# Kernel tuning notes

Hardware: AMD Instinct MI355X
Metric: run time of the kernel (lower is better)

Reference implementation:

```python
import jax, jax.numpy as jnp
import numpy as np

N_X = 50000      # real nodes
N_MOTIF = 10000  # motif nodes
N = N_X + N_MOTIF
E = 1_920_000    # edges (avg degree 32)
NFEAT = 512
NHID = 256
PAD_N = 65536


def setup_inputs() -> dict:
    key = jax.random.key(0)
    ks = jax.random.split(key, 12)
    x = jax.random.normal(ks[0], (N_X, NFEAT), dtype=jnp.float32)
    motif_emb = jax.random.normal(ks[1], (N_MOTIF, NFEAT), dtype=jnp.float32)
    adj_rows = jax.random.randint(ks[2], (E,), 0, N)
    adj_cols = jax.random.randint(ks[3], (E,), 0, N)
    adj_vals = jax.random.uniform(ks[4], (E,), dtype=jnp.float32)
    # unique scatter positions (torch output[pos_idx]=x with distinct indices)
    pos_idx = jax.random.permutation(ks[5], PAD_N)[:N_X]
    # GraphConvolution params (pygcn style: support = x@W; out = spmm(adj, support) + b)
    s1 = 1.0 / np.sqrt(NHID)
    w1 = jax.random.uniform(ks[6], (NFEAT, NHID), minval=-s1, maxval=s1, dtype=jnp.float32)
    b1 = jax.random.uniform(ks[7], (NHID,), minval=-s1, maxval=s1, dtype=jnp.float32)
    w2 = jax.random.uniform(ks[8], (NHID, NHID), minval=-s1, maxval=s1, dtype=jnp.float32)
    b2 = jax.random.uniform(ks[9], (NHID,), minval=-s1, maxval=s1, dtype=jnp.float32)
    w3 = jax.random.uniform(ks[10], (NHID, NHID), minval=-s1, maxval=s1, dtype=jnp.float32)
    b3 = jax.random.uniform(ks[11], (NHID,), minval=-s1, maxval=s1, dtype=jnp.float32)
    return {"x": x, "motif_emb": motif_emb, "adj_rows": adj_rows, "adj_cols": adj_cols,
            "adj_vals": adj_vals, "pos_idx": pos_idx, "pad_n": PAD_N,
            "w1": w1, "b1": b1, "w2": w2, "b2": b2, "w3": w3, "b3": b3}


def _gcn_layer(h, rows, cols, vals, w, b):
    support = h @ w                                   # [N, nhid]
    msgs = vals[:, None] * support[cols]              # [E, nhid]
    agg = jax.ops.segment_sum(msgs, rows, num_segments=N)  # spmm(adj, support)
    return jax.nn.relu(agg + b)


def reference(x, motif_emb, adj_rows, adj_cols, adj_vals, pos_idx, pad_n,
              w1, b1, w2, b2, w3, b3):
    h = jnp.concatenate((x, motif_emb), axis=0)       # [N, nfeat]
    h = _gcn_layer(h, adj_rows, adj_cols, adj_vals, w1, b1)
    # dropout is identity in eval mode
    h = _gcn_layer(h, adj_rows, adj_cols, adj_vals, w2, b2)
    h = _gcn_layer(h, adj_rows, adj_cols, adj_vals, w3, b3)
    h = h[:N_X]                                       # drop motif nodes
    output = jnp.zeros((pad_n, h.shape[1]), dtype=h.dtype)
    output = output.at[pos_idx].set(h)                # irregular scatter-assign
    return output
```

## Files before the change

kernel.cpp:

```cpp
#include <hip/hip_runtime.h>

#define N_TOTAL 60000
#define N_X     50000
#define N_EDGE  1920000
#define NFEAT   512
#define NHID    256
#define SLOTS   96

typedef __attribute__((ext_vector_type(8))) short bf16x8;
typedef __attribute__((ext_vector_type(4))) float f32x4;
typedef __attribute__((ext_vector_type(4))) unsigned u32x4;

__device__ __forceinline__ unsigned short f2bf(float f) {
    unsigned u = __float_as_uint(f);
    unsigned r = (u + 0x7FFFu + ((u >> 16) & 1u)) >> 16;
    return (unsigned short)r;
}
__device__ __forceinline__ float bf_lo(unsigned u) { return __uint_as_float(u << 16); }
__device__ __forceinline__ float bf_hi(unsigned u) { return __uint_as_float(u & 0xFFFF0000u); }

__global__ __launch_bounds__(256)
void cvt_w_all_kernel(const float* __restrict__ w1, const float* __restrict__ w2,
                      const float* __restrict__ w3, short* __restrict__ w1T,
                      short* __restrict__ w2T, short* __restrict__ w3T)
{
    int n = blockIdx.x;
    for (int k = threadIdx.x; k < NFEAT; k += 256)
        w1T[(size_t)n * NFEAT + k] = (short)f2bf(w1[(size_t)k * NHID + n]);
    for (int k = threadIdx.x; k < NHID; k += 256)
        w2T[(size_t)n * NHID + k] = (short)f2bf(w2[(size_t)k * NHID + n]);
    for (int k = threadIdx.x; k < NHID; k += 256)
        w3T[(size_t)n * NHID + k] = (short)f2bf(w3[(size_t)k * NHID + n]);
}

#define LDA 40

template<bool AF32>
__global__ __launch_bounds__(256)
void gemm_bt_kernel(const float* __restrict__ Af, const float* __restrict__ A2f, int split,
                    const short* __restrict__ Ab, const short* __restrict__ BT,
                    short* __restrict__ C, int M, int K)
{
    __shared__ short As[128 * LDA];
    __shared__ short Bs[128 * LDA];
    const int t    = threadIdx.x;
    const int lane = t & 63;
    const int wave = t >> 6;
    const int wm   = wave & 1;
    const int wn   = wave >> 1;
    const int l16  = lane & 15;
    const int quad = lane >> 4;
    const int bm   = blockIdx.x * 128;
    const int bn   = blockIdx.y * 128;

    f32x4 acc[4][4] = {};

    const int srow = t >> 2;
    const int sch  = t & 3;
    const int frow = t >> 1;
    const int fh   = t & 1;

    for (int kk = 0; kk < K; kk += 32) {
        if (AF32) {
            int row = bm + frow;
            float4 v0 = {}, v1 = {}, v2 = {}, v3 = {};
            if (row < M) {
                const float* src = (row < split) ? (Af + (size_t)row * K)
                                                 : (A2f + (size_t)(row - split) * K);
                const float4* p = (const float4*)(src + kk + fh * 16);
                v0 = p[0]; v1 = p[1]; v2 = p[2]; v3 = p[3];
            }
            short* dst = &As[frow * LDA + fh * 16];
            short tmp[16] = {
                (short)f2bf(v0.x), (short)f2bf(v0.y), (short)f2bf(v0.z), (short)f2bf(v0.w),
                (short)f2bf(v1.x), (short)f2bf(v1.y), (short)f2bf(v1.z), (short)f2bf(v1.w),
                (short)f2bf(v2.x), (short)f2bf(v2.y), (short)f2bf(v2.z), (short)f2bf(v2.w),
                (short)f2bf(v3.x), (short)f2bf(v3.y), (short)f2bf(v3.z), (short)f2bf(v3.w)};
            *(bf16x8*)(dst)     = *(const bf16x8*)&tmp[0];
            *(bf16x8*)(dst + 8) = *(const bf16x8*)&tmp[8];
        } else {
            bf16x8 va0 = {}, va1 = {};
            int r0 = bm + srow, r1 = bm + srow + 64;
            if (r0 < M) va0 = *(const bf16x8*)(Ab + (size_t)r0 * K + kk + sch * 8);
            if (r1 < M) va1 = *(const bf16x8*)(Ab + (size_t)r1 * K + kk + sch * 8);
            *(bf16x8*)&As[srow * LDA + sch * 8]        = va0;
            *(bf16x8*)&As[(srow + 64) * LDA + sch * 8] = va1;
        }
        {
            bf16x8 vb0 = *(const bf16x8*)(BT + (size_t)(bn + srow) * K + kk + sch * 8);
            bf16x8 vb1 = *(const bf16x8*)(BT + (size_t)(bn + srow + 64) * K + kk + sch * 8);
            *(bf16x8*)&Bs[srow * LDA + sch * 8]        = vb0;
            *(bf16x8*)&Bs[(srow + 64) * LDA + sch * 8] = vb1;
        }
        __syncthreads();

        bf16x8 af[4], bfr[4];
        #pragma unroll
        for (int i = 0; i < 4; i++) {
            af[i]  = *(const bf16x8*)&As[(wm * 64 + i * 16 + l16) * LDA + quad * 8];
            bfr[i] = *(const bf16x8*)&Bs[(wn * 64 + i * 16 + l16) * LDA + quad * 8];
        }
        #pragma unroll
        for (int i = 0; i < 4; i++)
            #pragma unroll
            for (int j = 0; j < 4; j++)
                acc[i][j] = __builtin_amdgcn_mfma_f32_16x16x32_bf16(af[i], bfr[j], acc[i][j], 0, 0, 0);
        __syncthreads();
    }

    #pragma unroll
    for (int i = 0; i < 4; i++) {
        #pragma unroll
        for (int r = 0; r < 4; r++) {
            int row = bm + wm * 64 + i * 16 + quad * 4 + r;
            if (row < M) {
                #pragma unroll
                for (int j = 0; j < 4; j++) {
                    int col = bn + wn * 64 + j * 16 + l16;
                    __builtin_nontemporal_store((short)f2bf(acc[i][j][r]),
                                                C + (size_t)row * NHID + col);
                }
            }
        }
    }
}

__global__ __launch_bounds__(256)
void init_cursor_kernel(int* __restrict__ cursor)
{
    int i = blockIdx.x * 256 + threadIdx.x;
    if (i < N_TOTAL) cursor[i] = i * SLOTS;
}

__global__ __launch_bounds__(256)
void scatter_edges_kernel(const int* __restrict__ rows, const int* __restrict__ cols,
                          const float* __restrict__ vals, int* __restrict__ cursor,
                          unsigned* __restrict__ edges)
{
    const int b = blockIdx.x;
    const int g = b & 7;
    const int i = (b >> 3) * 256 + threadIdx.x;
    const int lo = g * (N_TOTAL / 8);
    const int hi = lo + (N_TOTAL / 8);
    int r = __builtin_nontemporal_load(&rows[i]);
    if (r >= lo && r < hi) {
        unsigned rec = (unsigned)cols[i] | ((unsigned)f2bf(vals[i]) << 16);
        int p = atomicAdd(&cursor[r], 1);
        edges[p] = rec;
    }
}

template<int MODE>
__global__ __launch_bounds__(256)
void spmm_relu_kernel(const int* __restrict__ row_end, const unsigned* __restrict__ edges,
                      const u32x4* __restrict__ support, const float* __restrict__ bias,
                      u32x4* __restrict__ out_bf, float* __restrict__ out_f32,
                      const int* __restrict__ pos, int nrows)
{
    __shared__ unsigned s_edge[4][64];
    const int wave = threadIdx.x >> 6;
    const int lane = threadIdx.x & 63;
    const int r    = blockIdx.x * 4 + wave;
    if (r >= nrows) return;
    const int eh = lane >> 5;
    const int fl = lane & 31;
    const int start = r * SLOTS;
    const int end   = row_end[r];
    const u32x4* __restrict__ sb = support + fl;

    float a[8] = {}, b2[8] = {};
    for (int base = start; base < end; base += 64) {
        int j = base + lane;
        asm volatile("s_waitcnt lgkmcnt(0)" ::: "memory");
        if (j < end) s_edge[wave][lane] = __builtin_nontemporal_load(&edges[j]);
        asm volatile("s_waitcnt lgkmcnt(0)" ::: "memory");
        __builtin_amdgcn_sched_barrier(0);
        int cnt = min(64, end - base);
        int i = eh;
        for (; i + 6 < cnt; i += 8) {
            unsigned e0 = s_edge[wave][i];
            unsigned e1 = s_edge[wave][i + 2];
            unsigned e2 = s_edge[wave][i + 4];
            unsigned e3 = s_edge[wave][i + 6];
            u32x4 u0 = sb[(size_t)(e0 & 0xFFFFu) * 32];
            u32x4 u1 = sb[(size_t)(e1 & 0xFFFFu) * 32];
            u32x4 u2 = sb[(size_t)(e2 & 0xFFFFu) * 32];
            u32x4 u3 = sb[(size_t)(e3 & 0xFFFFu) * 32];
            float v0 = bf_hi(e0), v1 = bf_hi(e1), v2 = bf_hi(e2), v3 = bf_hi(e3);
            #pragma unroll
            for (int k = 0; k < 4; k++) {
                a[2*k]      += v0 * bf_lo(u0[k]);
                a[2*k + 1]  += v0 * bf_hi(u0[k]);
                b2[2*k]     += v1 * bf_lo(u1[k]);
                b2[2*k + 1] += v1 * bf_hi(u1[k]);
            }
            #pragma unroll
            for (int k = 0; k < 4; k++) {
                a[2*k]      += v2 * bf_lo(u2[k]);
                a[2*k + 1]  += v2 * bf_hi(u2[k]);
                b2[2*k]     += v3 * bf_lo(u3[k]);
                b2[2*k + 1] += v3 * bf_hi(u3[k]);
            }
        }
        for (; i + 2 < cnt; i += 4) {
            unsigned e0 = s_edge[wave][i], e1 = s_edge[wave][i + 2];
            u32x4 u0 = sb[(size_t)(e0 & 0xFFFFu) * 32];
            u32x4 u1 = sb[(size_t)(e1 & 0xFFFFu) * 32];
            float v0 = bf_hi(e0), v1 = bf_hi(e1);
            #pragma unroll
            for (int k = 0; k < 4; k++) {
                a[2*k]      += v0 * bf_lo(u0[k]);
                a[2*k + 1]  += v0 * bf_hi(u0[k]);
                b2[2*k]     += v1 * bf_lo(u1[k]);
                b2[2*k + 1] += v1 * bf_hi(u1[k]);
            }
        }
        for (; i < cnt; i += 2) {
            unsigned e0 = s_edge[wave][i];
            u32x4 u0 = sb[(size_t)(e0 & 0xFFFFu) * 32];
            float v0 = bf_hi(e0);
            #pragma unroll
            for (int k = 0; k < 4; k++) {
                a[2*k]     += v0 * bf_lo(u0[k]);
                a[2*k + 1] += v0 * bf_hi(u0[k]);
            }
        }
    }

    const f32x4* bb = (const f32x4*)bias + fl * 2;
    f32x4 bv0 = bb[0], bv1 = bb[1];
    float o[8];
    #pragma unroll
    for (int k = 0; k < 8; k++) {
        float s = a[k] + b2[k];
        s += __shfl_xor(s, 32, 64);
        float bk = (k < 4) ? bv0[k] : bv1[k - 4];
        o[k] = fmaxf(s + bk, 0.f);
    }
    if (lane < 32) {
        if (MODE == 1) {
            f32x4 q0 = {o[0], o[1], o[2], o[3]};
            f32x4 q1 = {o[4], o[5], o[6], o[7]};
            f32x4* dst = (f32x4*)out_f32 + (size_t)pos[r] * 64 + fl * 2;
            __builtin_nontemporal_store(q0, dst);
            __builtin_nontemporal_store(q1, dst + 1);
        } else {
            u32x4 q;
            #pragma unroll
            for (int k = 0; k < 4; k++)
                q[k] = (unsigned)f2bf(o[2*k]) | ((unsigned)f2bf(o[2*k + 1]) << 16);
            __builtin_nontemporal_store(q, out_bf + (size_t)r * 32 + fl);
        }
    }
}

extern "C" void kernel_launch(void* const* d_in, const int* in_sizes, int n_in,
                              void* d_out, int out_size, void* d_ws, size_t ws_size,
                              hipStream_t stream)
{
    const float* x     = (const float*)d_in[0];
    const float* motif = (const float*)d_in[1];
    const int*   rows  = (const int*)d_in[2];
    const int*   cols  = (const int*)d_in[3];
    const float* vals  = (const float*)d_in[4];
    const int*   pos   = (const int*)d_in[5];
    const float* w1 = (const float*)d_in[7];
    const float* b1 = (const float*)d_in[8];
    const float* w2 = (const float*)d_in[9];
    const float* b2 = (const float*)d_in[10];
    const float* w3 = (const float*)d_in[11];
    const float* b3 = (const float*)d_in[12];
    (void)ws_size; (void)n_in; (void)in_sizes;

    char* ws = (char*)d_ws;
    size_t off = 0;
    short* h_bf     = (short*)(ws + off); off += (size_t)N_TOTAL * NHID * 2;
    short* support  = (short*)(ws + off); off += (size_t)N_TOTAL * NHID * 2;
    short* w1T      = (short*)(ws + off); off += (size_t)NHID * NFEAT * 2;
    short* w2T      = (short*)(ws + off); off += (size_t)NHID * NHID * 2;
    short* w3T      = (short*)(ws + off); off += (size_t)NHID * NHID * 2;
    int* cursor     = (int*)(ws + off);   off += 60032 * 4;
    unsigned* edges = (unsigned*)(ws + off); off += (size_t)N_TOTAL * SLOTS * 4;

    hipMemsetAsync(d_out, 0, (size_t)out_size * sizeof(float), stream);
    cvt_w_all_kernel<<<NHID, 256, 0, stream>>>(w1, w2, w3, w1T, w2T, w3T);
    init_cursor_kernel<<<(N_TOTAL + 255) / 256, 256, 0, stream>>>(cursor);
    scatter_edges_kernel<<<(N_EDGE / 256) * 8, 256, 0, stream>>>(rows, cols, vals, cursor, edges);

    dim3 ggrid((N_TOTAL + 127) / 128, NHID / 128);

    gemm_bt_kernel<true><<<ggrid, 256, 0, stream>>>(x, motif, N_X, nullptr, w1T, support, N_TOTAL, NFEAT);
    spmm_relu_kernel<0><<<(N_TOTAL + 3) / 4, 256, 0, stream>>>(cursor, edges, (const u32x4*)support, b1,
                                                               (u32x4*)h_bf, nullptr, nullptr, N_TOTAL);
    gemm_bt_kernel<false><<<ggrid, 256, 0, stream>>>(nullptr, nullptr, 0, h_bf, w2T, support, N_TOTAL, NHID);
    spmm_relu_kernel<0><<<(N_TOTAL + 3) / 4, 256, 0, stream>>>(cursor, edges, (const u32x4*)support, b2,
                                                               (u32x4*)h_bf, nullptr, nullptr, N_TOTAL);
    gemm_bt_kernel<false><<<ggrid, 256, 0, stream>>>(nullptr, nullptr, 0, h_bf, w3T, support, N_TOTAL, NHID);
    spmm_relu_kernel<1><<<(N_X + 3) / 4, 256, 0, stream>>>(cursor, edges, (const u32x4*)support, b3,
                                                           nullptr, (float*)d_out, pos, N_X);
}
```

Measured before the change: 743.9 us.

## Store support in column-chunked layout and split SpMM feature dimension across blocks

The GEMM output is written in a chunked layout, 8 column chunks of 32 features each, with every chunk stored contiguously per row. The SpMM now launches 8 blocks per row group. Each block handles one 32-feature chunk, with 16 edge lanes times 4 feature lanes per wave and a shuffle reduction at the end. The aim is to make the gathered support working set per chunk small enough to fit in cache, at the cost of 8x more reads of edge lists and 64-byte gathers instead of 512-byte ones.

```diff
diff --git a/kernel.cpp b/kernel.cpp
--- a/kernel.cpp
+++ b/kernel.cpp
@@ -6,6 +6,7 @@
 #define NFEAT   512
 #define NHID    256
 #define SLOTS   96
+#define NCHUNK  8
 
 typedef __attribute__((ext_vector_type(8))) short bf16x8;
 typedef __attribute__((ext_vector_type(4))) float f32x4;
@@ -117,8 +118,8 @@
                 #pragma unroll
                 for (int j = 0; j < 4; j++) {
                     int col = bn + wn * 64 + j * 16 + l16;
-                    __builtin_nontemporal_store((short)f2bf(acc[i][j][r]),
-                                                C + (size_t)row * NHID + col);
+                    size_t idx = (size_t)(col >> 5) * M * 32 + (size_t)row * 32 + (col & 31);
+                    __builtin_nontemporal_store((short)f2bf(acc[i][j][r]), C + idx);
                 }
             }
         }
@@ -153,22 +154,24 @@
 template<int MODE>
 __global__ __launch_bounds__(256)
 void spmm_relu_kernel(const int* __restrict__ row_end, const unsigned* __restrict__ edges,
-                      const u32x4* __restrict__ support, const float* __restrict__ bias,
+                      const u32x4* __restrict__ supportC, const float* __restrict__ bias,
                       u32x4* __restrict__ out_bf, float* __restrict__ out_f32,
                       const int* __restrict__ pos, int nrows)
 {
     __shared__ unsigned s_edge[4][64];
-    const int wave = threadIdx.x >> 6;
-    const int lane = threadIdx.x & 63;
-    const int r    = blockIdx.x * 4 + wave;
+    const int chunk = blockIdx.x & 7;
+    const int grp   = blockIdx.x >> 3;
+    const int wave  = threadIdx.x >> 6;
+    const int lane  = threadIdx.x & 63;
+    const int r     = grp * 4 + wave;
     if (r >= nrows) return;
-    const int eh = lane >> 5;
-    const int fl = lane & 31;
+    const int eh = lane >> 2;
+    const int fl = lane & 3;
     const int start = r * SLOTS;
     const int end   = row_end[r];
-    const u32x4* __restrict__ sb = support + fl;
-
-    float a[8] = {}, b2[8] = {};
+    const u32x4* __restrict__ sb = supportC + (size_t)chunk * N_TOTAL * 4 + fl;
+
+    float a[8] = {};
     for (int base = start; base < end; base += 64) {
         int j = base + lane;
         asm volatile("s_waitcnt lgkmcnt(0)" ::: "memory");
@@ -177,47 +180,41 @@
         __builtin_amdgcn_sched_barrier(0);
         int cnt = min(64, end - base);
         int i = eh;
-        for (; i + 6 < cnt; i += 8) {
+        if (i + 48 < cnt) {
             unsigned e0 = s_edge[wave][i];
-            unsigned e1 = s_edge[wave][i + 2];
-            unsigned e2 = s_edge[wave][i + 4];
-            unsigned e3 = s_edge[wave][i + 6];
-            u32x4 u0 = sb[(size_t)(e0 & 0xFFFFu) * 32];
-            u32x4 u1 = sb[(size_t)(e1 & 0xFFFFu) * 32];
-            u32x4 u2 = sb[(size_t)(e2 & 0xFFFFu) * 32];
-            u32x4 u3 = sb[(size_t)(e3 & 0xFFFFu) * 32];
+            unsigned e1 = s_edge[wave][i + 16];
+            unsigned e2 = s_edge[wave][i + 32];
+            unsigned e3 = s_edge[wave][i + 48];
+            u32x4 u0 = sb[(size_t)(e0 & 0xFFFFu) * 4];
+            u32x4 u1 = sb[(size_t)(e1 & 0xFFFFu) * 4];
+            u32x4 u2 = sb[(size_t)(e2 & 0xFFFFu) * 4];
+            u32x4 u3 = sb[(size_t)(e3 & 0xFFFFu) * 4];
             float v0 = bf_hi(e0), v1 = bf_hi(e1), v2 = bf_hi(e2), v3 = bf_hi(e3);
             #pragma unroll
             for (int k = 0; k < 4; k++) {
-                a[2*k]      += v0 * bf_lo(u0[k]);
-                a[2*k + 1]  += v0 * bf_hi(u0[k]);
-                b2[2*k]     += v1 * bf_lo(u1[k]);
-                b2[2*k + 1] += v1 * bf_hi(u1[k]);
-            }
+                a[2*k]     += v0 * bf_lo(u0[k]) + v1 * bf_lo(u1[k]);
+                a[2*k + 1] += v0 * bf_hi(u0[k]) + v1 * bf_hi(u1[k]);
+                a[2*k]     += v2 * bf_lo(u2[k]) + v3 * bf_lo(u3[k]);
+                a[2*k + 1] += v2 * bf_hi(u2[k]) + v3 * bf_hi(u3[k]);
+            }
+            i += 64;
+        }
+        if (i + 16 < cnt) {
+            unsigned e0 = s_edge[wave][i];
+            unsigned e1 = s_edge[wave][i + 16];
+            u32x4 u0 = sb[(size_t)(e0 & 0xFFFFu) * 4];
+            u32x4 u1 = sb[(size_t)(e1 & 0xFFFFu) * 4];
+            float v0 = bf_hi(e0), v1 = bf_hi(e1);
             #pragma unroll
             for (int k = 0; k < 4; k++) {
-                a[2*k]      += v2 * bf_lo(u2[k]);
-                a[2*k + 1]  += v2 * bf_hi(u2[k]);
-                b2[2*k]     += v3 * bf_lo(u3[k]);
-                b2[2*k + 1] += v3 * bf_hi(u3[k]);
-            }
-        }
-        for (; i + 2 < cnt; i += 4) {
-            unsigned e0 = s_edge[wave][i], e1 = s_edge[wave][i + 2];
-            u32x4 u0 = sb[(size_t)(e0 & 0xFFFFu) * 32];
-            u32x4 u1 = sb[(size_t)(e1 & 0xFFFFu) * 32];
-            float v0 = bf_hi(e0), v1 = bf_hi(e1);
-            #pragma unroll
-            for (int k = 0; k < 4; k++) {
-                a[2*k]      += v0 * bf_lo(u0[k]);
-                a[2*k + 1]  += v0 * bf_hi(u0[k]);
-                b2[2*k]     += v1 * bf_lo(u1[k]);
-                b2[2*k + 1] += v1 * bf_hi(u1[k]);
-            }
-        }
-        for (; i < cnt; i += 2) {
+                a[2*k]     += v0 * bf_lo(u0[k]) + v1 * bf_lo(u1[k]);
+                a[2*k + 1] += v0 * bf_hi(u0[k]) + v1 * bf_hi(u1[k]);
+            }
+            i += 32;
+        }
+        if (i < cnt) {
             unsigned e0 = s_edge[wave][i];
-            u32x4 u0 = sb[(size_t)(e0 & 0xFFFFu) * 32];
+            u32x4 u0 = sb[(size_t)(e0 & 0xFFFFu) * 4];
             float v0 = bf_hi(e0);
             #pragma unroll
             for (int k = 0; k < 4; k++) {
@@ -227,21 +224,24 @@
         }
     }
 
-    const f32x4* bb = (const f32x4*)bias + fl * 2;
+    const f32x4* bb = (const f32x4*)bias + chunk * 8 + fl * 2;
     f32x4 bv0 = bb[0], bv1 = bb[1];
     float o[8];
     #pragma unroll
     for (int k = 0; k < 8; k++) {
-        float s = a[k] + b2[k];
+        float s = a[k];
+        s += __shfl_xor(s, 4, 64);
+        s += __shfl_xor(s, 8, 64);
+        s += __shfl_xor(s, 16, 64);
         s += __shfl_xor(s, 32, 64);
         float bk = (k < 4) ? bv0[k] : bv1[k - 4];
         o[k] = fmaxf(s + bk, 0.f);
     }
-    if (lane < 32) {
+    if (lane < 4) {
         if (MODE == 1) {
             f32x4 q0 = {o[0], o[1], o[2], o[3]};
             f32x4 q1 = {o[4], o[5], o[6], o[7]};
-            f32x4* dst = (f32x4*)out_f32 + (size_t)pos[r] * 64 + fl * 2;
+            f32x4* dst = (f32x4*)out_f32 + (size_t)pos[r] * 64 + chunk * 8 + fl * 2;
             __builtin_nontemporal_store(q0, dst);
             __builtin_nontemporal_store(q1, dst + 1);
         } else {
@@ -249,7 +249,7 @@
             #pragma unroll
             for (int k = 0; k < 4; k++)
                 q[k] = (unsigned)f2bf(o[2*k]) | ((unsigned)f2bf(o[2*k + 1]) << 16);
-            __builtin_nontemporal_store(q, out_bf + (size_t)r * 32 + fl);
+            __builtin_nontemporal_store(q, out_bf + (size_t)r * 32 + chunk * 4 + fl);
         }
     }
 }
@@ -288,14 +288,16 @@
     scatter_edges_kernel<<<(N_EDGE / 256) * 8, 256, 0, stream>>>(rows, cols, vals, cursor, edges);
 
     dim3 ggrid((N_TOTAL + 127) / 128, NHID / 128);
+    const int sgrid0 = ((N_TOTAL + 3) / 4) * NCHUNK;
+    const int sgrid1 = ((N_X + 3) / 4) * NCHUNK;
 
     gemm_bt_kernel<true><<<ggrid, 256, 0, stream>>>(x, motif, N_X, nullptr, w1T, support, N_TOTAL, NFEAT);
-    spmm_relu_kernel<0><<<(N_TOTAL + 3) / 4, 256, 0, stream>>>(cursor, edges, (const u32x4*)support, b1,
-                                                               (u32x4*)h_bf, nullptr, nullptr, N_TOTAL);
+    spmm_relu_kernel<0><<<sgrid0, 256, 0, stream>>>(cursor, edges, (const u32x4*)support, b1,
+                                                    (u32x4*)h_bf, nullptr, nullptr, N_TOTAL);
     gemm_bt_kernel<false><<<ggrid, 256, 0, stream>>>(nullptr, nullptr, 0, h_bf, w2T, support, N_TOTAL, NHID);
-    spmm_relu_kernel<0><<<(N_TOTAL + 3) / 4, 256, 0, stream>>>(cursor, edges, (const u32x4*)support, b2,
-                                                               (u32x4*)h_bf, nullptr, nullptr, N_TOTAL);
+    spmm_relu_kernel<0><<<sgrid0, 256, 0, stream>>>(cursor, edges, (const u32x4*)support, b2,
+                                                    (u32x4*)h_bf, nullptr, nullptr, N_TOTAL);
     gemm_bt_kernel<false><<<ggrid, 256, 0, stream>>>(nullptr, nullptr, 0, h_bf, w3T, support, N_TOTAL, NHID);
-    spmm_relu_kernel<1><<<(N_X + 3) / 4, 256, 0, stream>>>(cursor, edges, (const u32x4*)support, b3,
-                                                           nullptr, (float*)d_out, pos, N_X);
-}
+    spmm_relu_kernel<1><<<sgrid1, 256, 0, stream>>>(cursor, edges, (const u32x4*)support, b3,
+                                                    nullptr, (float*)d_out, pos, N_X);
+}
```

Measured after the change: 1.010 ms. +35.8%, slower.
